# Performance work log

Hardware: AMD Instinct MI355X
Metric: run time of the kernel (lower is better)

Reference implementation:

```python
import jax, jax.numpy as jnp
import numpy as np

B, N, IN_DIM, DIM, KNN = 8, 2048, 128, 128, 16
POS_H = 64
ATTN_H = DIM * 4
EPS = 1e-5
SCALE = 1.0 / np.sqrt(DIM).astype(np.float32)


def setup_inputs() -> dict:
    key = jax.random.key(0)
    ks = jax.random.split(key, 10)
    nrm = lambda k, shape, s=0.02: jax.random.normal(k, shape, jnp.float32) * s
    return dict(
        ori_x=jax.random.normal(ks[0], (B, N, IN_DIM), jnp.float32),
        pos=jax.random.normal(ks[1], (B, N, 3), jnp.float32),
        w_in=nrm(ks[2], (IN_DIM, DIM)),
        w_qkv=nrm(ks[3], (DIM, 3 * DIM)),
        w_out=nrm(ks[4], (DIM, IN_DIM)),
        pos_w1=nrm(ks[5], (3, POS_H)), pos_b1=jnp.zeros((POS_H,), jnp.float32),
        pos_bn_g=jnp.ones((POS_H,), jnp.float32), pos_bn_b=jnp.zeros((POS_H,), jnp.float32),
        pos_bn_m=jnp.zeros((POS_H,), jnp.float32), pos_bn_v=jnp.ones((POS_H,), jnp.float32),
        pos_w2=nrm(ks[6], (POS_H, DIM)), pos_b2=jnp.zeros((DIM,), jnp.float32),
        attn_w1=nrm(ks[7], (DIM, ATTN_H)), attn_b1=jnp.zeros((ATTN_H,), jnp.float32),
        attn_bn_g=jnp.ones((ATTN_H,), jnp.float32), attn_bn_b=jnp.zeros((ATTN_H,), jnp.float32),
        attn_bn_m=jnp.zeros((ATTN_H,), jnp.float32), attn_bn_v=jnp.ones((ATTN_H,), jnp.float32),
        attn_w2=nrm(ks[8], (ATTN_H, DIM)), attn_b2=jnp.zeros((DIM,), jnp.float32),
    )


def _bn_eval(x, g, b, m, v):
    # BatchNorm2d in eval mode; channel is the last axis in our [b,n,k,C] layout
    return (x - m) * (g * jax.lax.rsqrt(v + EPS)) + b


def reference(ori_x, pos, w_in, w_qkv, w_out,
              pos_w1, pos_b1, pos_bn_g, pos_bn_b, pos_bn_m, pos_bn_v, pos_w2, pos_b2,
              attn_w1, attn_b1, attn_bn_g, attn_bn_b, attn_bn_m, attn_bn_v, attn_w2, attn_b2):
    x = ori_x @ w_in                                  # [b,n,dim]
    qkv = x @ w_qkv
    q, k, v = jnp.split(qkv, 3, axis=-1)              # each [b,n,dim]

    # pairwise squared distances [b,n,n] (monotone in rel_dist -> same topk)
    sq = jnp.sum(pos * pos, axis=-1)
    d2 = sq[:, :, None] + sq[:, None, :] - 2.0 * jnp.einsum('bnd,bmd->bnm', pos, pos)
    _, idx = jax.lax.top_k(-d2, KNN)                  # [b,n,KNN] nearest neighbors

    gather = jax.vmap(lambda t, i: t[i])              # [n,C],[n,k] -> [n,k,C] per batch
    k_g = gather(k, idx)                              # [b,n,k,dim]
    v_g = gather(v, idx)
    pos_g = gather(pos, idx)                          # [b,n,k,3]

    rel_pos = pos[:, :, None, :] - pos_g              # [b,n,k,3]
    pe = jax.nn.relu(_bn_eval(rel_pos @ pos_w1 + pos_b1, pos_bn_g, pos_bn_b, pos_bn_m, pos_bn_v))
    pe = pe @ pos_w2 + pos_b2                         # [b,n,k,dim]

    qk_rel = q[:, :, None, :] - k_g                   # [b,n,k,dim]
    h = jax.nn.relu(_bn_eval((qk_rel + pe) @ attn_w1 + attn_b1,
                             attn_bn_g, attn_bn_b, attn_bn_m, attn_bn_v))
    h = h @ attn_w2 + attn_b2                         # [b,n,k,dim]

    attn = jax.nn.softmax(h * SCALE, axis=-2)         # softmax over neighbors
    agg = jnp.sum(attn * (v_g + pe), axis=2)          # [b,n,dim]
    return agg @ w_out + ori_x
```

## Files before the change

### kernel.cpp

```cpp
#include <hip/hip_runtime.h>

#define EPS 1e-5f

constexpr int NB   = 8;
constexpr int NN   = 2048;
constexpr int DIM  = 128;
constexpr int KNN  = 16;
constexpr int AH   = 512;
constexpr int NPTS = NB * NN;
constexpr float SCALE = 0.08838834764831845f;

typedef __attribute__((ext_vector_type(8))) short short8;
typedef __attribute__((ext_vector_type(4))) float floatx4;

__device__ __forceinline__ short f2bf(float f) {
  union { float f; unsigned u; } a; a.f = f;
  return (short)((a.u + 0x8000u) >> 16);
}
__device__ __forceinline__ float bf2f(short s) {
  union { unsigned u; float f; } a; a.u = ((unsigned)(unsigned short)s) << 16;
  return a.f;
}

__global__ __launch_bounds__(256) void gemm_f32(
    const float* __restrict__ A, const float* __restrict__ W,
    float* __restrict__ C, int M, int N, int K)
{
  __shared__ float As[64][33];
  __shared__ float Ws[32][65];
  const int bm = blockIdx.x * 64, bn = blockIdx.y * 64;
  const int tid = threadIdx.x;
  const int tx = tid & 15, ty = tid >> 4;
  float acc[4][4] = {};
  for (int k0 = 0; k0 < K; k0 += 32) {
#pragma unroll
    for (int i = 0; i < 8; ++i) {
      int e = tid + i * 256;
      As[e >> 5][e & 31] = A[(size_t)(bm + (e >> 5)) * K + k0 + (e & 31)];
    }
#pragma unroll
    for (int i = 0; i < 8; ++i) {
      int e = tid + i * 256;
      Ws[e >> 6][e & 63] = W[(size_t)(k0 + (e >> 6)) * N + bn + (e & 63)];
    }
    __syncthreads();
#pragma unroll
    for (int kk = 0; kk < 32; ++kk) {
      float a[4], w[4];
#pragma unroll
      for (int i = 0; i < 4; ++i) a[i] = As[ty * 4 + i][kk];
#pragma unroll
      for (int j = 0; j < 4; ++j) w[j] = Ws[kk][tx * 4 + j];
#pragma unroll
      for (int i = 0; i < 4; ++i)
#pragma unroll
        for (int j = 0; j < 4; ++j)
          acc[i][j] += a[i] * w[j];
    }
    __syncthreads();
  }
#pragma unroll
  for (int i = 0; i < 4; ++i)
#pragma unroll
    for (int j = 0; j < 4; ++j)
      C[(size_t)(bm + ty * 4 + i) * N + bn + tx * 4 + j] = acc[i][j];
}

__global__ __launch_bounds__(256) void knn_kernel(
    const float* __restrict__ pos_t, int* __restrict__ idx_out)
{
  const int tid = threadIdx.x;
  const int lane = tid & 63;
  const int p = blockIdx.x * 4 + (tid >> 6);
  const int b = p >> 11, i = p & (NN - 1);
  const float* px = pos_t + (size_t)b * 3 * NN;
  const float* py = px + NN;
  const float* pz = py + NN;
  const float xi = px[i], yi = py[i], zi = pz[i];
  const float sqi = xi * xi + yi * yi + zi * zi;
  float v[32];
#pragma unroll
  for (int t = 0; t < 32; ++t) {
    int j = t * 64 + lane;
    float xj = px[j], yj = py[j], zj = pz[j];
    float sqj = xj * xj + yj * yj + zj * zj;
    float dot = xi * xj + yi * yj + zi * zj;
    v[t] = sqi + sqj - 2.0f * dot;
  }
  for (int s = 0; s < KNN; ++s) {
    float bv = 3.4e38f; int bj = 1 << 30;
#pragma unroll
    for (int t = 0; t < 32; ++t) {
      if (v[t] < bv) { bv = v[t]; bj = t * 64 + lane; }
    }
#pragma unroll
    for (int m = 1; m < 64; m <<= 1) {
      float ov = __shfl_xor(bv, m);
      int   oj = __shfl_xor(bj, m);
      if (ov < bv || (ov == bv && oj < bj)) { bv = ov; bj = oj; }
    }
    if (lane == 0) idx_out[(size_t)p * KNN + s] = bj;
#pragma unroll
    for (int t = 0; t < 32; ++t)
      if (bj == t * 64 + lane) v[t] = 3.4e38f;
  }
}

__global__ __launch_bounds__(256) void pack_weights(
    const float* __restrict__ attn_w1, const float* __restrict__ attn_w2,
    const float* __restrict__ pos_w2, const float* __restrict__ Wf,
    const float* __restrict__ w_out, const float* __restrict__ pos,
    const float* __restrict__ attn_b1, const float* __restrict__ abn_g,
    const float* __restrict__ abn_b, const float* __restrict__ abn_m,
    const float* __restrict__ abn_v,
    const float* __restrict__ pos_b1, const float* __restrict__ pbn_g,
    const float* __restrict__ pbn_b, const float* __restrict__ pbn_m,
    const float* __restrict__ pbn_v, const float* __restrict__ pos_b2,
    short* __restrict__ w1p, short* __restrict__ w2p, short* __restrict__ pw2p,
    short* __restrict__ wfp, short* __restrict__ wop,
    float* __restrict__ biasq,
    float* __restrict__ t1sc, float* __restrict__ t1bi,
    float* __restrict__ phsc, float* __restrict__ phbi,
    float* __restrict__ pos_t)
{
  int t = blockIdx.x * 256 + threadIdx.x;
  if (t < 65536) {
    int j = t & 7, lane = (t >> 3) & 63, ks = (t >> 9) & 3, nt = (t >> 11) & 3, ch = t >> 13;
    int q = lane >> 4, cc = lane & 15;
    int k = ks * 32 + q * 8 + j, n = ch * 64 + nt * 16 + cc;
    w1p[t] = f2bf(attn_w1[(size_t)k * AH + n]);
  } else if (t < 131072) {
    int e = t - 65536;
    int j = e & 7, lane = (e >> 3) & 63, ks = (e >> 9) & 1, nt = (e >> 10) & 7, ch = e >> 13;
    int q = lane >> 4, cc = lane & 15;
    int k = ch * 64 + ks * 32 + q * 8 + j, n = nt * 16 + cc;
    w2p[e] = f2bf(attn_w2[(size_t)k * DIM + n]);
  } else if (t < 139264) {
    int e = t - 131072;
    int j = e & 7, lane = (e >> 3) & 63, ks = (e >> 9) & 1, nt = e >> 10;
    int q = lane >> 4, cc = lane & 15;
    int k = ks * 32 + q * 8 + j, n = nt * 16 + cc;
    pw2p[e] = f2bf(pos_w2[(size_t)k * DIM + n]);
  } else if (t < 188416) {
    int e = t - 139264;
    int j = e & 7, lane = (e >> 3) & 63, ks = (e >> 9) & 3, nt = (e >> 11) & 7, nc = e >> 14;
    int q = lane >> 4, cc = lane & 15;
    int k = ks * 32 + q * 8 + j, n = nc * 128 + nt * 16 + cc;
    wfp[e] = f2bf(Wf[(size_t)k * 384 + n]);
  } else if (t < 204800) {
    int e = t - 188416;
    int j = e & 7, lane = (e >> 3) & 63, ks = (e >> 9) & 3, nt = (e >> 11) & 7;
    int q = lane >> 4, cc = lane & 15;
    int k = ks * 32 + q * 8 + j, n = nt * 16 + cc;
    wop[e] = f2bf(w_out[(size_t)k * DIM + n]);
  } else if (t < 205184) {
    int c = t - 204800;
    biasq[c] = (c < 128) ? pos_b2[c] : ((c < 256) ? 0.0f : pos_b2[c - 256]);
  } else if (t < 205696) {
    int c = t - 205184;
    t1sc[c] = abn_g[c] * rsqrtf(abn_v[c] + EPS);
  } else if (t < 206208) {
    int c = t - 205696;
    float sc = abn_g[c] * rsqrtf(abn_v[c] + EPS);
    t1bi[c] = (attn_b1[c] - abn_m[c]) * sc + abn_b[c];
  } else if (t < 206272) {
    int c = t - 206208;
    phsc[c] = pbn_g[c] * rsqrtf(pbn_v[c] + EPS);
  } else if (t < 206336) {
    int c = t - 206272;
    float sc = pbn_g[c] * rsqrtf(pbn_v[c] + EPS);
    phbi[c] = (pos_b1[c] - pbn_m[c]) * sc + pbn_b[c];
  } else if (t < 206336 + NPTS * 3) {
    int e = t - 206336;
    int p = e / 3, d = e - p * 3;
    int b = p >> 11, n = p & (NN - 1);
    pos_t[((size_t)b * 3 + d) * NN + n] = pos[e];
  }
}

__global__ __launch_bounds__(256, 4) void gemm_in(
    const float* __restrict__ A, const short* __restrict__ wfp,
    const float* __restrict__ biasq, short* __restrict__ C)
{
  __shared__ short As[64 * 128];
  const int tid = threadIdx.x;
  const int lane = tid & 63, w = tid >> 6;
  const int wr = w >> 1, wc = w & 1;
  const int q = lane >> 4, cc = lane & 15;
  const int row0 = blockIdx.x * 64;
#pragma unroll
  for (int it = 0; it < 4; ++it) {
    int e = tid + it * 256;
    int row = e >> 4, cg = e & 15;
    const float* src = A + (size_t)(row0 + row) * 128 + cg * 8;
    float4 f0 = *(const float4*)src, f1 = *(const float4*)(src + 4);
    short8 v;
    v[0] = f2bf(f0.x); v[1] = f2bf(f0.y); v[2] = f2bf(f0.z); v[3] = f2bf(f0.w);
    v[4] = f2bf(f1.x); v[5] = f2bf(f1.y); v[6] = f2bf(f1.z); v[7] = f2bf(f1.w);
    *(short8*)(As + row * 128 + ((cg ^ (row & 15)) << 3)) = v;
  }
  __syncthreads();
  for (int nc = 0; nc < 3; ++nc) {
    floatx4 acc[2][4];
#pragma unroll
    for (int i = 0; i < 2; ++i)
#pragma unroll
      for (int jt = 0; jt < 4; ++jt) acc[i][jt] = (floatx4){0.f, 0.f, 0.f, 0.f};
#pragma unroll
    for (int ks = 0; ks < 4; ++ks) {
      short8 a8[2], b8[4];
#pragma unroll
      for (int i = 0; i < 2; ++i) {
        int row = (wr * 2 + i) * 16 + cc;
        a8[i] = *(const short8*)(As + row * 128 + (((ks * 4 + q) ^ cc) << 3));
      }
#pragma unroll
      for (int jt = 0; jt < 4; ++jt)
        b8[jt] = *(const short8*)(wfp + ((((nc * 8 + wc * 4 + jt) * 4 + ks) * 64 + lane) << 3));
#pragma unroll
      for (int i = 0; i < 2; ++i)
#pragma unroll
        for (int jt = 0; jt < 4; ++jt)
          acc[i][jt] = __builtin_amdgcn_mfma_f32_16x16x32_bf16(a8[i], b8[jt], acc[i][jt], 0, 0, 0);
    }
#pragma unroll
    for (int jt = 0; jt < 4; ++jt) {
      int colG = nc * 128 + (wc * 4 + jt) * 16 + cc;
      float bv = biasq[colG];
#pragma unroll
      for (int i = 0; i < 2; ++i)
#pragma unroll
        for (int r = 0; r < 4; ++r) {
          int row = (wr * 2 + i) * 16 + q * 4 + r;
          C[(size_t)(row0 + row) * 384 + colG] = f2bf(acc[i][jt][r] + bv);
        }
    }
  }
}

__global__ __launch_bounds__(256, 4) void gemm_out(
    const float* __restrict__ A, const short* __restrict__ wop,
    const float* __restrict__ R, float* __restrict__ C)
{
  __shared__ short As[64 * 128];
  const int tid = threadIdx.x;
  const int lane = tid & 63, w = tid >> 6;
  const int wr = w >> 1, wc = w & 1;
  const int q = lane >> 4, cc = lane & 15;
  const int row0 = blockIdx.x * 64;
#pragma unroll
  for (int it = 0; it < 4; ++it) {
    int e = tid + it * 256;
    int row = e >> 4, cg = e & 15;
    const float* src = A + (size_t)(row0 + row) * 128 + cg * 8;
    float4 f0 = *(const float4*)src, f1 = *(const float4*)(src + 4);
    short8 v;
    v[0] = f2bf(f0.x); v[1] = f2bf(f0.y); v[2] = f2bf(f0.z); v[3] = f2bf(f0.w);
    v[4] = f2bf(f1.x); v[5] = f2bf(f1.y); v[6] = f2bf(f1.z); v[7] = f2bf(f1.w);
    *(short8*)(As + row * 128 + ((cg ^ (row & 15)) << 3)) = v;
  }
  __syncthreads();
  floatx4 acc[2][4];
#pragma unroll
  for (int i = 0; i < 2; ++i)
#pragma unroll
    for (int jt = 0; jt < 4; ++jt) acc[i][jt] = (floatx4){0.f, 0.f, 0.f, 0.f};
#pragma unroll
  for (int ks = 0; ks < 4; ++ks) {
    short8 a8[2], b8[4];
#pragma unroll
    for (int i = 0; i < 2; ++i) {
      int row = (wr * 2 + i) * 16 + cc;
      a8[i] = *(const short8*)(As + row * 128 + (((ks * 4 + q) ^ cc) << 3));
    }
#pragma unroll
    for (int jt = 0; jt < 4; ++jt)
      b8[jt] = *(const short8*)(wop + ((((wc * 4 + jt) * 4 + ks) * 64 + lane) << 3));
#pragma unroll
    for (int i = 0; i < 2; ++i)
#pragma unroll
      for (int jt = 0; jt < 4; ++jt)
        acc[i][jt] = __builtin_amdgcn_mfma_f32_16x16x32_bf16(a8[i], b8[jt], acc[i][jt], 0, 0, 0);
  }
#pragma unroll
  for (int jt = 0; jt < 4; ++jt) {
    int col = (wc * 4 + jt) * 16 + cc;
#pragma unroll
    for (int i = 0; i < 2; ++i)
#pragma unroll
      for (int r = 0; r < 4; ++r) {
        int row = (wr * 2 + i) * 16 + q * 4 + r;
        size_t o = (size_t)(row0 + row) * 128 + col;
        C[o] = acc[i][jt][r] + R[o];
      }
  }
}

__global__ __launch_bounds__(256, 3) void fused_attn(
    const float* __restrict__ pos, const short* __restrict__ qkv,
    const int* __restrict__ knn_idx,
    const float* __restrict__ pos_w1,
    const short* __restrict__ w1p, const short* __restrict__ w2p,
    const short* __restrict__ pw2p,
    const float* __restrict__ t1sc, const float* __restrict__ t1bi,
    const float* __restrict__ phsc, const float* __restrict__ phbi,
    const float* __restrict__ attn_b2,
    float* __restrict__ agg)
{
  __shared__ short av_s[64 * 128];
  __shared__ short t1_s[64 * 64];
  __shared__ short q_ss[4 * 128];
  __shared__ float relp_s[64 * 4];
  __shared__ int   nbr_s[64];

  const int tid = threadIdx.x;
  const int lane = tid & 63, w = tid >> 6;
  const int wr = w >> 1, wc = w & 1;
  const int q = lane >> 4, cc = lane & 15;
  const int bb = blockIdx.x & 7;
  const int gp0 = bb * NN + (blockIdx.x >> 3) * 4;

  if (tid < 64) nbr_s[tid] = knn_idx[(size_t)gp0 * KNN + tid];
  if (tid >= 64 && tid < 128) {
    int e = tid - 64;
    int p = e >> 4, seg = e & 15;
    *(short8*)(q_ss + p * 128 + seg * 8) =
        *(const short8*)(qkv + (size_t)(gp0 + p) * 384 + seg * 8);
  }
  __syncthreads();
  if (tid < 64) {
    int p = tid >> 4;
    int j = nbr_s[tid];
    const float* pa = pos + (size_t)(gp0 + p) * 3;
    const float* pj = pos + ((size_t)bb * NN + j) * 3;
    relp_s[tid * 4 + 0] = pa[0] - pj[0];
    relp_s[tid * 4 + 1] = pa[1] - pj[1];
    relp_s[tid * 4 + 2] = pa[2] - pj[2];
  }
  __syncthreads();

#pragma unroll
  for (int r2 = 0; r2 < 16; ++r2) {
    int e = tid + r2 * 256;
    int row = e >> 6, c = e & 63;
    float lin = relp_s[row * 4] * pos_w1[c] + relp_s[row * 4 + 1] * pos_w1[64 + c]
              + relp_s[row * 4 + 2] * pos_w1[128 + c];
    t1_s[row * 64 + (((c >> 3) ^ (row & 7)) << 3) + (c & 7)] =
        f2bf(fmaxf(lin * phsc[c] + phbi[c], 0.0f));
  }
  __syncthreads();

  floatx4 pe[2][4];
#pragma unroll
  for (int i = 0; i < 2; ++i)
#pragma unroll
    for (int jt = 0; jt < 4; ++jt) pe[i][jt] = (floatx4){0.f, 0.f, 0.f, 0.f};
#pragma unroll
  for (int ks = 0; ks < 2; ++ks) {
    short8 a8[2];
#pragma unroll
    for (int i = 0; i < 2; ++i) {
      int row = (wr * 2 + i) * 16 + cc;
      a8[i] = *(const short8*)(t1_s + row * 64 + (((ks * 4 + q) ^ (row & 7)) << 3));
    }
#pragma unroll
    for (int jt = 0; jt < 4; ++jt) {
      short8 b8 = *(const short8*)(pw2p + ((((wc * 4 + jt) * 2 + ks) * 64 + lane) << 3));
#pragma unroll
      for (int i = 0; i < 2; ++i)
        pe[i][jt] = __builtin_amdgcn_mfma_f32_16x16x32_bf16(a8[i], b8, pe[i][jt], 0, 0, 0);
    }
  }

  float qreg[2][4];
#pragma unroll
  for (int i = 0; i < 2; ++i)
#pragma unroll
    for (int jt = 0; jt < 4; ++jt)
      qreg[i][jt] = bf2f(q_ss[(wr * 2 + i) * 128 + (wc * 4 + jt) * 16 + cc]);

  floatx4 vpe[2][4];
#pragma unroll
  for (int i = 0; i < 2; ++i) {
    int rt = wr * 2 + i;
#pragma unroll
    for (int r = 0; r < 4; ++r) {
      int row = rt * 16 + q * 4 + r;
      const short* kv = qkv + ((size_t)bb * NN + nbr_s[row]) * 384;
      int sb = row * 128, sx = row & 15;
#pragma unroll
      for (int jt = 0; jt < 4; ++jt) {
        int col = (wc * 4 + jt) * 16 + cc;
        float pev = pe[i][jt][r];
        av_s[sb + (((col >> 3) ^ sx) << 3) + (col & 7)] =
            f2bf(qreg[i][jt] - bf2f(kv[128 + col]) + pev);
        vpe[i][jt][r] = bf2f(kv[256 + col]) + pev;
      }
    }
  }
  __syncthreads();

  short8 af[2][4];
#pragma unroll
  for (int i = 0; i < 2; ++i) {
    int row = (wr * 2 + i) * 16 + cc;
#pragma unroll
    for (int ks = 0; ks < 4; ++ks)
      af[i][ks] = *(const short8*)(av_s + row * 128 + (((ks * 4 + q) ^ cc) << 3));
  }
  __syncthreads();

#pragma unroll
  for (int i = 0; i < 2; ++i) {
    int rt = wr * 2 + i;
#pragma unroll
    for (int r = 0; r < 4; ++r) {
      int row = rt * 16 + q * 4 + r;
      int sb = row * 128, sx = row & 15;
#pragma unroll
      for (int jt = 0; jt < 4; ++jt) {
        int col = (wc * 4 + jt) * 16 + cc;
        av_s[sb + (((col >> 3) ^ sx) << 3) + (col & 7)] = f2bf(vpe[i][jt][r]);
      }
    }
  }

  floatx4 hacc[2][4];
#pragma unroll
  for (int i = 0; i < 2; ++i)
#pragma unroll
    for (int jt = 0; jt < 4; ++jt) hacc[i][jt] = (floatx4){0.f, 0.f, 0.f, 0.f};

  for (int ch = 0; ch < 8; ++ch) {
#pragma unroll
    for (int jt = 0; jt < 2; ++jt) {
      floatx4 tacc[2];
      tacc[0] = (floatx4){0.f, 0.f, 0.f, 0.f};
      tacc[1] = (floatx4){0.f, 0.f, 0.f, 0.f};
#pragma unroll
      for (int ks = 0; ks < 4; ++ks) {
        short8 b8 = *(const short8*)(w1p + ((((ch * 4 + wc * 2 + jt) * 4 + ks) * 64 + lane) << 3));
#pragma unroll
        for (int i = 0; i < 2; ++i)
          tacc[i] = __builtin_amdgcn_mfma_f32_16x16x32_bf16(af[i][ks], b8, tacc[i], 0, 0, 0);
      }
      int colL = (wc * 2 + jt) * 16 + cc;
      int colG = ch * 64 + colL;
      float sc = t1sc[colG], bi = t1bi[colG];
#pragma unroll
      for (int i = 0; i < 2; ++i)
#pragma unroll
        for (int r = 0; r < 4; ++r) {
          int row = (wr * 2 + i) * 16 + q * 4 + r;
          t1_s[row * 64 + (((colL >> 3) ^ (row & 7)) << 3) + (colL & 7)] =
              f2bf(fmaxf(tacc[i][r] * sc + bi, 0.0f));
        }
    }
    __syncthreads();
#pragma unroll
    for (int ks = 0; ks < 2; ++ks) {
      short8 a8[2];
#pragma unroll
      for (int i = 0; i < 2; ++i) {
        int row = (wr * 2 + i) * 16 + cc;
        a8[i] = *(const short8*)(t1_s + row * 64 + (((ks * 4 + q) ^ (row & 7)) << 3));
      }
#pragma unroll
      for (int jh = 0; jh < 2; ++jh) {
        short8 b8[2];
#pragma unroll
        for (int j2 = 0; j2 < 2; ++j2)
          b8[j2] = *(const short8*)(w2p + ((((ch * 8 + wc * 4 + jh * 2 + j2) * 2 + ks) * 64 + lane) << 3));
#pragma unroll
        for (int i = 0; i < 2; ++i)
#pragma unroll
          for (int j2 = 0; j2 < 2; ++j2)
            hacc[i][jh * 2 + j2] = __builtin_amdgcn_mfma_f32_16x16x32_bf16(a8[i], b8[j2], hacc[i][jh * 2 + j2], 0, 0, 0);
      }
    }
    __syncthreads();
  }

#pragma unroll
  for (int i = 0; i < 2; ++i) {
    int rt = wr * 2 + i;
#pragma unroll
    for (int jt = 0; jt < 4; ++jt) {
      int col = (wc * 4 + jt) * 16 + cc;
      float b2v = attn_b2[col];
      float v0[4], mx = -3.4e38f;
#pragma unroll
      for (int r = 0; r < 4; ++r) {
        v0[r] = (hacc[i][jt][r] + b2v) * SCALE;
        mx = fmaxf(mx, v0[r]);
      }
      mx = fmaxf(mx, __shfl_xor(mx, 16));
      mx = fmaxf(mx, __shfl_xor(mx, 32));
      float ex[4], sum = 0.f;
#pragma unroll
      for (int r = 0; r < 4; ++r) { ex[r] = __expf(v0[r] - mx); sum += ex[r]; }
      sum += __shfl_xor(sum, 16);
      sum += __shfl_xor(sum, 32);
      float inv = 1.0f / sum;
      float part = 0.f;
#pragma unroll
      for (int r = 0; r < 4; ++r) {
        int row = rt * 16 + q * 4 + r;
        int slot = row * 128 + (((col >> 3) ^ (row & 15)) << 3) + (col & 7);
        part += ex[r] * bf2f(av_s[slot]);
      }
      part += __shfl_xor(part, 16);
      part += __shfl_xor(part, 32);
      if (q == 0) agg[(size_t)(gp0 + rt) * DIM + col] = part * inv;
    }
  }
}

extern "C" void kernel_launch(void* const* d_in, const int* in_sizes, int n_in,
                              void* d_out, int out_size, void* d_ws, size_t ws_size,
                              hipStream_t stream)
{
  const float* ori_x    = (const float*)d_in[0];
  const float* pos      = (const float*)d_in[1];
  const float* w_in     = (const float*)d_in[2];
  const float* w_qkv    = (const float*)d_in[3];
  const float* w_out    = (const float*)d_in[4];
  const float* pos_w1   = (const float*)d_in[5];
  const float* pos_b1   = (const float*)d_in[6];
  const float* pos_bn_g = (const float*)d_in[7];
  const float* pos_bn_b = (const float*)d_in[8];
  const float* pos_bn_m = (const float*)d_in[9];
  const float* pos_bn_v = (const float*)d_in[10];
  const float* pos_w2   = (const float*)d_in[11];
  const float* pos_b2   = (const float*)d_in[12];
  const float* attn_w1  = (const float*)d_in[13];
  const float* attn_b1  = (const float*)d_in[14];
  const float* attn_bn_g = (const float*)d_in[15];
  const float* attn_bn_b = (const float*)d_in[16];
  const float* attn_bn_m = (const float*)d_in[17];
  const float* attn_bn_v = (const float*)d_in[18];
  const float* attn_w2  = (const float*)d_in[19];
  const float* attn_b2  = (const float*)d_in[20];
  float* out = (float*)d_out;

  float* agg  = (float*)d_ws;
  float* Wf   = agg;
  short* qkvb = (short*)(agg + (size_t)NPTS * DIM);
  int*   idx  = (int*)(qkvb + (size_t)NPTS * 3 * DIM);
  short* w1p  = (short*)(idx + (size_t)NPTS * KNN);
  short* w2p  = w1p + 65536;
  short* pw2p = w2p + 65536;
  short* wfp  = pw2p + 8192;
  short* wop  = wfp + 49152;
  float* biasq = (float*)(wop + 16384);
  float* t1sc = biasq + 384;
  float* t1bi = t1sc + 512;
  float* phsc = t1bi + 512;
  float* phbi = phsc + 64;
  float* pos_t = phbi + 64;

  gemm_f32<<<dim3(2, 6), 256, 0, stream>>>(w_in, w_qkv, Wf, 128, 384, 128);
  pack_weights<<<998, 256, 0, stream>>>(attn_w1, attn_w2, pos_w2, Wf, w_out, pos,
      attn_b1, attn_bn_g, attn_bn_b, attn_bn_m, attn_bn_v,
      pos_b1, pos_bn_g, pos_bn_b, pos_bn_m, pos_bn_v, pos_b2,
      w1p, w2p, pw2p, wfp, wop, biasq, t1sc, t1bi, phsc, phbi, pos_t);
  gemm_in<<<NPTS / 64, 256, 0, stream>>>(ori_x, wfp, biasq, qkvb);
  knn_kernel<<<NPTS / 4, 256, 0, stream>>>(pos_t, idx);
  fused_attn<<<NPTS / 4, 256, 0, stream>>>(pos, qkvb, idx, pos_w1,
      w1p, w2p, pw2p, t1sc, t1bi, phsc, phbi, attn_b2, agg);
  gemm_out<<<NPTS / 64, 256, 0, stream>>>(agg, wop, ori_x, out);
}
```

Measured before the change: 345.4 us.

## Fuse KNN selection into attention kernel and split qkv GEMM columns across grid

The separate KNN kernel is removed. Each wave of fused_attn now computes distances and top-16 selection for its own point, and writes the neighbor indices and relative positions straight to shared memory, so the index buffer round-trip and one launch go away. gemm_in is also split across a second grid dimension over the three 128-column chunks, which gives more blocks but converts the tile to bf16 three times. The KNN work now sits inside the attention kernel with its 32-float register array, which may raise register pressure and lower occupancy under launch_bounds(256,3).

```diff
diff --git a/kernel.cpp b/kernel.cpp
--- a/kernel.cpp
+++ b/kernel.cpp
@@ -64,46 +64,6 @@
 #pragma unroll
     for (int j = 0; j < 4; ++j)
       C[(size_t)(bm + ty * 4 + i) * N + bn + tx * 4 + j] = acc[i][j];
-}
-
-__global__ __launch_bounds__(256) void knn_kernel(
-    const float* __restrict__ pos_t, int* __restrict__ idx_out)
-{
-  const int tid = threadIdx.x;
-  const int lane = tid & 63;
-  const int p = blockIdx.x * 4 + (tid >> 6);
-  const int b = p >> 11, i = p & (NN - 1);
-  const float* px = pos_t + (size_t)b * 3 * NN;
-  const float* py = px + NN;
-  const float* pz = py + NN;
-  const float xi = px[i], yi = py[i], zi = pz[i];
-  const float sqi = xi * xi + yi * yi + zi * zi;
-  float v[32];
-#pragma unroll
-  for (int t = 0; t < 32; ++t) {
-    int j = t * 64 + lane;
-    float xj = px[j], yj = py[j], zj = pz[j];
-    float sqj = xj * xj + yj * yj + zj * zj;
-    float dot = xi * xj + yi * yj + zi * zj;
-    v[t] = sqi + sqj - 2.0f * dot;
-  }
-  for (int s = 0; s < KNN; ++s) {
-    float bv = 3.4e38f; int bj = 1 << 30;
-#pragma unroll
-    for (int t = 0; t < 32; ++t) {
-      if (v[t] < bv) { bv = v[t]; bj = t * 64 + lane; }
-    }
-#pragma unroll
-    for (int m = 1; m < 64; m <<= 1) {
-      float ov = __shfl_xor(bv, m);
-      int   oj = __shfl_xor(bj, m);
-      if (ov < bv || (ov == bv && oj < bj)) { bv = ov; bj = oj; }
-    }
-    if (lane == 0) idx_out[(size_t)p * KNN + s] = bj;
-#pragma unroll
-    for (int t = 0; t < 32; ++t)
-      if (bj == t * 64 + lane) v[t] = 3.4e38f;
-  }
 }
 
 __global__ __launch_bounds__(256) void pack_weights(
@@ -188,6 +148,7 @@
   const int wr = w >> 1, wc = w & 1;
   const int q = lane >> 4, cc = lane & 15;
   const int row0 = blockIdx.x * 64;
+  const int nc = blockIdx.y;
 #pragma unroll
   for (int it = 0; it < 4; ++it) {
     int e = tid + it * 256;
@@ -200,41 +161,39 @@
     *(short8*)(As + row * 128 + ((cg ^ (row & 15)) << 3)) = v;
   }
   __syncthreads();
-  for (int nc = 0; nc < 3; ++nc) {
-    floatx4 acc[2][4];
+  floatx4 acc[2][4];
+#pragma unroll
+  for (int i = 0; i < 2; ++i)
+#pragma unroll
+    for (int jt = 0; jt < 4; ++jt) acc[i][jt] = (floatx4){0.f, 0.f, 0.f, 0.f};
+#pragma unroll
+  for (int ks = 0; ks < 4; ++ks) {
+    short8 a8[2], b8[4];
+#pragma unroll
+    for (int i = 0; i < 2; ++i) {
+      int row = (wr * 2 + i) * 16 + cc;
+      a8[i] = *(const short8*)(As + row * 128 + (((ks * 4 + q) ^ cc) << 3));
+    }
+#pragma unroll
+    for (int jt = 0; jt < 4; ++jt)
+      b8[jt] = *(const short8*)(wfp + ((((nc * 8 + wc * 4 + jt) * 4 + ks) * 64 + lane) << 3));
 #pragma unroll
     for (int i = 0; i < 2; ++i)
 #pragma unroll
-      for (int jt = 0; jt < 4; ++jt) acc[i][jt] = (floatx4){0.f, 0.f, 0.f, 0.f};
-#pragma unroll
-    for (int ks = 0; ks < 4; ++ks) {
-      short8 a8[2], b8[4];
-#pragma unroll
-      for (int i = 0; i < 2; ++i) {
-        int row = (wr * 2 + i) * 16 + cc;
-        a8[i] = *(const short8*)(As + row * 128 + (((ks * 4 + q) ^ cc) << 3));
-      }
-#pragma unroll
       for (int jt = 0; jt < 4; ++jt)
-        b8[jt] = *(const short8*)(wfp + ((((nc * 8 + wc * 4 + jt) * 4 + ks) * 64 + lane) << 3));
-#pragma unroll
-      for (int i = 0; i < 2; ++i)
-#pragma unroll
-        for (int jt = 0; jt < 4; ++jt)
-          acc[i][jt] = __builtin_amdgcn_mfma_f32_16x16x32_bf16(a8[i], b8[jt], acc[i][jt], 0, 0, 0);
-    }
-#pragma unroll
-    for (int jt = 0; jt < 4; ++jt) {
-      int colG = nc * 128 + (wc * 4 + jt) * 16 + cc;
-      float bv = biasq[colG];
-#pragma unroll
-      for (int i = 0; i < 2; ++i)
-#pragma unroll
-        for (int r = 0; r < 4; ++r) {
-          int row = (wr * 2 + i) * 16 + q * 4 + r;
-          C[(size_t)(row0 + row) * 384 + colG] = f2bf(acc[i][jt][r] + bv);
-        }
-    }
+        acc[i][jt] = __builtin_amdgcn_mfma_f32_16x16x32_bf16(a8[i], b8[jt], acc[i][jt], 0, 0, 0);
+  }
+#pragma unroll
+  for (int jt = 0; jt < 4; ++jt) {
+    int colG = nc * 128 + (wc * 4 + jt) * 16 + cc;
+    float bv = biasq[colG];
+#pragma unroll
+    for (int i = 0; i < 2; ++i)
+#pragma unroll
+      for (int r = 0; r < 4; ++r) {
+        int row = (wr * 2 + i) * 16 + q * 4 + r;
+        C[(size_t)(row0 + row) * 384 + colG] = f2bf(acc[i][jt][r] + bv);
+      }
   }
 }
 
@@ -297,8 +256,7 @@
 }
 
 __global__ __launch_bounds__(256, 3) void fused_attn(
-    const float* __restrict__ pos, const short* __restrict__ qkv,
-    const int* __restrict__ knn_idx,
+    const float* __restrict__ pos_t, const short* __restrict__ qkv,
     const float* __restrict__ pos_w1,
     const short* __restrict__ w1p, const short* __restrict__ w2p,
     const short* __restrict__ pw2p,
@@ -318,24 +276,56 @@
   const int wr = w >> 1, wc = w & 1;
   const int q = lane >> 4, cc = lane & 15;
   const int bb = blockIdx.x & 7;
-  const int gp0 = bb * NN + (blockIdx.x >> 3) * 4;
-
-  if (tid < 64) nbr_s[tid] = knn_idx[(size_t)gp0 * KNN + tid];
+  const int ip0 = (blockIdx.x >> 3) * 4;
+  const int gp0 = bb * NN + ip0;
+
   if (tid >= 64 && tid < 128) {
     int e = tid - 64;
     int p = e >> 4, seg = e & 15;
     *(short8*)(q_ss + p * 128 + seg * 8) =
         *(const short8*)(qkv + (size_t)(gp0 + p) * 384 + seg * 8);
   }
-  __syncthreads();
-  if (tid < 64) {
-    int p = tid >> 4;
-    int j = nbr_s[tid];
-    const float* pa = pos + (size_t)(gp0 + p) * 3;
-    const float* pj = pos + ((size_t)bb * NN + j) * 3;
-    relp_s[tid * 4 + 0] = pa[0] - pj[0];
-    relp_s[tid * 4 + 1] = pa[1] - pj[1];
-    relp_s[tid * 4 + 2] = pa[2] - pj[2];
+
+  {
+    const float* px = pos_t + (size_t)bb * 3 * NN;
+    const float* py = px + NN;
+    const float* pz = py + NN;
+    const int ip = ip0 + w;
+    const float xi = px[ip], yi = py[ip], zi = pz[ip];
+    const float sqi = xi * xi + yi * yi + zi * zi;
+    float v[32];
+#pragma unroll
+    for (int t = 0; t < 32; ++t) {
+      int j = t * 64 + lane;
+      float xj = px[j], yj = py[j], zj = pz[j];
+      float sqj = xj * xj + yj * yj + zj * zj;
+      float dot = xi * xj + yi * yj + zi * zj;
+      v[t] = sqi + sqj - 2.0f * dot;
+    }
+    int mynbr = 0;
+    for (int s = 0; s < KNN; ++s) {
+      float bv = 3.4e38f; int bj = 1 << 30;
+#pragma unroll
+      for (int t = 0; t < 32; ++t) {
+        if (v[t] < bv) { bv = v[t]; bj = t * 64 + lane; }
+      }
+#pragma unroll
+      for (int m = 1; m < 64; m <<= 1) {
+        float ov = __shfl_xor(bv, m);
+        int   oj = __shfl_xor(bj, m);
+        if (ov < bv || (ov == bv && oj < bj)) { bv = ov; bj = oj; }
+      }
+      if (lane == s) mynbr = bj;
+#pragma unroll
+      for (int t = 0; t < 32; ++t)
+        if (bj == t * 64 + lane) v[t] = 3.4e38f;
+    }
+    if (lane < 16) {
+      nbr_s[w * 16 + lane] = mynbr;
+      relp_s[(w * 16 + lane) * 4 + 0] = xi - px[mynbr];
+      relp_s[(w * 16 + lane) * 4 + 1] = yi - py[mynbr];
+      relp_s[(w * 16 + lane) * 4 + 2] = zi - pz[mynbr];
+    }
   }
   __syncthreads();
 
@@ -546,8 +536,7 @@
   float* agg  = (float*)d_ws;
   float* Wf   = agg;
   short* qkvb = (short*)(agg + (size_t)NPTS * DIM);
-  int*   idx  = (int*)(qkvb + (size_t)NPTS * 3 * DIM);
-  short* w1p  = (short*)(idx + (size_t)NPTS * KNN);
+  short* w1p  = qkvb + (size_t)NPTS * 3 * DIM;
   short* w2p  = w1p + 65536;
   short* pw2p = w2p + 65536;
   short* wfp  = pw2p + 8192;
@@ -564,9 +553,8 @@
       attn_b1, attn_bn_g, attn_bn_b, attn_bn_m, attn_bn_v,
       pos_b1, pos_bn_g, pos_bn_b, pos_bn_m, pos_bn_v, pos_b2,
       w1p, w2p, pw2p, wfp, wop, biasq, t1sc, t1bi, phsc, phbi, pos_t);
-  gemm_in<<<NPTS / 64, 256, 0, stream>>>(ori_x, wfp, biasq, qkvb);
-  knn_kernel<<<NPTS / 4, 256, 0, stream>>>(pos_t, idx);
-  fused_attn<<<NPTS / 4, 256, 0, stream>>>(pos, qkvb, idx, pos_w1,
-      w1p, w2p, pw2p, t1sc, t1bi, phsc, phbi, attn_b2, agg);
+  gemm_in<<<dim3(NPTS / 64, 3), 256, 0, stream>>>(ori_x, wfp, biasq, qkvb);
+  fused_attn<<<NPTS / 4, 256, 0, stream>>>(pos_t, qkvb,
+      pos_w1, w1p, w2p, pw2p, t1sc, t1bi, phsc, phbi, attn_b2, agg);
   gemm_out<<<NPTS / 64, 256, 0, stream>>>(agg, wop, ori_x, out);
 }
```

Result: no change. 344.8 us (-0.2%).
